# Optimization experiments

Measured on AMD Instinct MI355X. Metric: run time of the kernel, lower is better.

Reference implementation:

```python
import jax, jax.numpy as jnp
import numpy as np

ALPHA1 = 0.1   # rank margin
ALPHA2 = 5.0   # penalty scale when violated
ALPHA3 = 10.0  # sigmoid sharpness
ALPHA_OTHER = 0.5  # floor for top-k threshold


def setup_inputs() -> dict:
    key = jax.random.key(0)
    B, C, L, S = 4096, 9605, 8, 50  # batch, classes, whitelist labels, classes per label
    k1, k2, k3 = jax.random.split(key, 3)
    x = jax.random.normal(k1, (B, C), dtype=jnp.float32)
    # sparse multi-label binarized targets (~10 positives/sample)
    y = (jax.random.uniform(k2, (B, C)) < 0.001).astype(jnp.float32)
    y_neg = (jax.random.uniform(k3, (B, C)) < 0.001).astype(jnp.float32)
    # disjoint per-label whitelist class index sets -> [L, C] boolean masks
    rng = np.random.default_rng(0)
    idx = rng.choice(C, size=L * S, replace=False).reshape(L, S)
    wl = np.zeros((L, C), dtype=bool)
    wl[np.arange(L)[:, None], idx] = True
    return {"x": x, "y": y, "y_neg": y_neg, "wl_mask": jnp.asarray(wl)}


def reference(x, y, y_neg, wl_mask):
    # x, y, y_neg: [B, C]; wl_mask: [L, C] bool. Returns scalar loss_rank_all.sum().
    # (The per-element BCE `loss` tensor and find_gt_whitelist(y_neg) in the
    #  original are dead code w.r.t. the returned value and are omitted.)
    xs = jax.nn.sigmoid(x)                                   # [B, C]
    wl_f = wl_mask.astype(x.dtype)                           # [L, C]
    # gt label present iff sum of y over that label's whitelist indices > 0
    gt_mask = (y @ wl_f.T) > 0                               # [B, L]
    has_gt = jnp.any(gt_mask, axis=1)                        # [B]
    first_gt = jnp.argmax(gt_mask, axis=1)                   # [B] first gt label
    # x_sorted[15] (16th largest) via top_k instead of full sort
    top16 = jax.lax.top_k(xs, 16)[0][:, 15]                  # [B]
    thres = jnp.maximum(top16, ALPHA_OTHER)                  # [B]
    # ---- branch: no gt whitelist label ----
    union = jnp.any(wl_mask, axis=0)                         # [C]
    x2_no = jnp.max(jnp.where(union[None, :], xs, -jnp.inf), axis=1)
    x1_no = thres
    # ---- branch: has gt whitelist label ----
    samp_mask = wl_mask[first_gt]                            # [B, C]
    x1_gt = jnp.max(jnp.where(samp_mask, xs, -jnp.inf), axis=1)
    L = wl_mask.shape[0]
    # faithful to original: indexes xs at LABEL positions 0..L-1, init 0
    non_gt = jnp.max(jnp.where(~gt_mask, xs[:, :L], 0.0), axis=1, initial=0.0)
    x2_gt = jnp.maximum(non_gt, thres)
    # ---- select branch and apply our_rank_loss ----
    x1 = jnp.where(has_gt, x1_gt, x1_no)
    x2 = jnp.where(has_gt, x2_gt, x2_no)
    d = x2 - x1 + ALPHA1
    sig = jax.nn.sigmoid(ALPHA3 * d)
    rank = jnp.where(d > 0, ALPHA2 * sig, sig)
    return jnp.sum(rank)
```

## Files before the change

kernel.cpp:

```cpp
#include <hip/hip_runtime.h>
#include <stdint.h>

#define BLOCK 512
#define NW 5
#define CAP 512
#define LISTCAP 1024
#define WS_LIST 8
#define WS_ROUT 4096
static constexpr int LBL = 8;

#define A1 0.1f
#define A2 5.0f
#define A3 10.0f

__device__ __forceinline__ unsigned f2key(float f) {
  unsigned u = __float_as_uint(f);
  return (u & 0x80000000u) ? ~u : (u | 0x80000000u);
}
__device__ __forceinline__ float key2f(unsigned k) {
  unsigned u = (k & 0x80000000u) ? (k & 0x7FFFFFFFu) : ~k;
  return __uint_as_float(u);
}
__device__ __forceinline__ float sigm(float v) { return 1.0f / (1.0f + __expf(-v)); }

__global__ void detect_kernel(const unsigned char* __restrict__ wl, int total,
                              int* __restrict__ ws) {
  int i = blockIdx.x * 256 + threadIdx.x;
  if (i < total && (i & 3) != 0 && wl[i] == 1) atomicOr(&ws[1], 1);
}

__global__ void build_kernel(const unsigned char* __restrict__ wl, int C, int total,
                             int* __restrict__ ws) {
  int i = blockIdx.x * 256 + threadIdx.x;
  if (i >= total) return;
  bool v = ws[1] ? (wl[i] != 0) : (((const int*)wl)[i] != 0);
  if (v) {
    int p = atomicAdd(&ws[0], 1);
    if (p < LISTCAP) ws[WS_LIST + p] = ((i / C) << 16) | (i % C);
  }
}

__global__ __launch_bounds__(BLOCK, 8) void rank_kernel(
    const float* __restrict__ x, const float* __restrict__ y,
    const int* __restrict__ ws, float* __restrict__ rout, int C) {
  __shared__ unsigned hist[2048];
  __shared__ unsigned buf[CAP];
  __shared__ float wtop2[BLOCK / 64];
  __shared__ unsigned wtot[BLOCK / 64];
  __shared__ unsigned lmaxk[LBL];
  __shared__ float smL[LBL];
  __shared__ unsigned gtbits, bufcnt, s_seld, s_selk, s_selc, s_key;

  int tid = threadIdx.x;
  int row = blockIdx.x;
  long long base = (long long)row * C;
  const float* __restrict__ xr = x + base;
  const float* __restrict__ yr = y + base;

  int s = (int)((4 - (base & 3)) & 3);
  int nv = (C - s) >> 2;
  int tail0 = s + 4 * nv;
  int nrem = C - 4 * nv;

  const float4* __restrict__ xv4 = (const float4*)(xr + s);
  float4 f[NW];
  bool hv[NW];
#pragma unroll
  for (int t = 0; t < NW; ++t) {
    int i = tid + t * BLOCK;
    hv[t] = (i < nv);
    f[t] = hv[t] ? xv4[i] : make_float4(-INFINITY, -INFINITY, -INFINITY, -INFINITY);
  }
  float tailv = -INFINITY;
  bool havet = false;
  if (tid < nrem) {
    int c = (tid < s) ? tid : tail0 + (tid - s);
    tailv = xr[c];
    havet = true;
  }
  if (tid < LBL) smL[tid] = xr[tid];
  int e0 = ws[WS_LIST + tid];
  int e1 = ws[WS_LIST + BLOCK + tid];
  float xg0 = 0.0f, yg0 = 0.0f, xg1 = 0.0f, yg1 = 0.0f;
  if (e0 != -1) { int c = e0 & 0xFFFF; xg0 = xr[c]; yg0 = yr[c]; }
  if (e1 != -1) { int c = e1 & 0xFFFF; xg1 = xr[c]; yg1 = yr[c]; }

  if (tid < LBL) lmaxk[tid] = 0u;
  if (tid == 0) { gtbits = 0u; bufcnt = 0u; }
  __syncthreads();

  if (e0 != -1) {
    int l = e0 >> 16;
    atomicMax(&lmaxk[l], f2key(xg0));
    if (yg0 != 0.0f) atomicOr(&gtbits, 1u << l);
  }
  if (e1 != -1) {
    int l = e1 >> 16;
    atomicMax(&lmaxk[l], f2key(xg1));
    if (yg1 != 0.0f) atomicOr(&gtbits, 1u << l);
  }

  float tmax = tailv;
#pragma unroll
  for (int t = 0; t < NW; ++t)
    tmax = fmaxf(tmax, fmaxf(fmaxf(f[t].x, f[t].y), fmaxf(f[t].z, f[t].w)));

  float a1 = tmax, a2 = -INFINITY;
#pragma unroll
  for (int st = 1; st < 64; st <<= 1) {
    float b1 = __shfl_xor(a1, st, 64);
    float b2 = __shfl_xor(a2, st, 64);
    float m = fminf(a1, b1);
    float o = (a1 >= b1) ? a2 : b2;
    a1 = fmaxf(a1, b1);
    a2 = fmaxf(m, o);
  }
  int w = tid >> 6;
  if ((tid & 63) == 0) wtop2[w] = a2;
  __syncthreads();
  float p = wtop2[0];
#pragma unroll
  for (int i = 1; i < BLOCK / 64; ++i) p = fminf(p, wtop2[i]);

#pragma unroll
  for (int t = 0; t < NW; ++t) {
    if (f[t].x >= p) { unsigned q = atomicAdd(&bufcnt, 1u); if (q < CAP) buf[q] = f2key(f[t].x); }
    if (f[t].y >= p) { unsigned q = atomicAdd(&bufcnt, 1u); if (q < CAP) buf[q] = f2key(f[t].y); }
    if (f[t].z >= p) { unsigned q = atomicAdd(&bufcnt, 1u); if (q < CAP) buf[q] = f2key(f[t].z); }
    if (f[t].w >= p) { unsigned q = atomicAdd(&bufcnt, 1u); if (q < CAP) buf[q] = f2key(f[t].w); }
  }
  if (havet && tailv >= p) { unsigned q = atomicAdd(&bufcnt, 1u); if (q < CAP) buf[q] = f2key(tailv); }
  __syncthreads();

  unsigned selkey = 0u;
  int bc = (int)bufcnt;
  if (bc >= 16 && bc <= CAP) {
    if (tid < 64) {
      for (int i = tid; i < bc; i += 64) {
        unsigned mk = buf[i];
        int g = 0, e2 = 0;
        for (int j = 0; j < bc; ++j) {
          unsigned bk = buf[j];
          g += (bk > mk);
          e2 += (bk == mk);
        }
        if (g < 16 && 16 <= g + e2) s_key = mk;
      }
    }
    __syncthreads();
    selkey = s_key;
  } else {
    unsigned prefix = 0, pmask = 0;
    int k = 16;
    bool done = false;
    const int SHa[3] = {21, 10, 0};
    const int WIDa[3] = {11, 11, 10};
    for (int lev = 0; lev < 3 && !done; ++lev) {
      int shift = SHa[lev];
      int nb = 1 << WIDa[lev];
      unsigned bmask = (unsigned)nb - 1u;
      for (int i = tid; i < nb; i += BLOCK) hist[i] = 0;
      if (tid == 0) bufcnt = 0;
      __syncthreads();
#pragma unroll
      for (int t = 0; t < NW; ++t)
        if (hv[t]) {
          unsigned kk[4] = {f2key(f[t].x), f2key(f[t].y), f2key(f[t].z), f2key(f[t].w)};
#pragma unroll
          for (int e = 0; e < 4; ++e)
            if ((kk[e] & pmask) == prefix) atomicAdd(&hist[(kk[e] >> shift) & bmask], 1u);
        }
      if (havet) {
        unsigned tk = f2key(tailv);
        if ((tk & pmask) == prefix) atomicAdd(&hist[(tk >> shift) & bmask], 1u);
      }
      __syncthreads();
      int bpt = nb / BLOCK;
      int b0 = tid * bpt;
      unsigned cs = 0;
      for (int b = 0; b < bpt; ++b) cs += hist[b0 + b];
      unsigned v = cs;
      int lane = tid & 63;
#pragma unroll
      for (int st = 1; st < 64; st <<= 1) {
        unsigned tv = __shfl_down(v, st, 64);
        if (lane + st < 64) v += tv;
      }
      int w2 = tid >> 6;
      if (lane == 0) wtot[w2] = v;
      __syncthreads();
      unsigned above = 0;
      for (int ww = w2 + 1; ww < BLOCK / 64; ++ww) above += wtot[ww];
      unsigned S_incl = v + above;
      unsigned S_excl = S_incl - cs;
      if (S_excl < (unsigned)k && (unsigned)k <= S_incl) {
        int kk2 = k - (int)S_excl;
        int d = b0 + bpt - 1;
        for (; d > b0; --d) {
          int cb = (int)hist[d];
          if (kk2 <= cb) break;
          kk2 -= cb;
        }
        s_seld = (unsigned)d;
        s_selk = (unsigned)kk2;
        s_selc = hist[d];
      }
      __syncthreads();
      prefix |= s_seld << shift;
      pmask |= bmask << shift;
      k = (int)s_selk;
      unsigned selc = s_selc;
      if (lev == 2) {
        selkey = prefix;
        done = true;
      } else if (selc <= (unsigned)CAP) {
#pragma unroll
        for (int t = 0; t < NW; ++t)
          if (hv[t]) {
            unsigned kk[4] = {f2key(f[t].x), f2key(f[t].y), f2key(f[t].z), f2key(f[t].w)};
#pragma unroll
            for (int e = 0; e < 4; ++e)
              if ((kk[e] & pmask) == prefix) {
                unsigned q = atomicAdd(&bufcnt, 1u);
                if (q < CAP) buf[q] = kk[e];
              }
          }
        if (havet) {
          unsigned tk = f2key(tailv);
          if ((tk & pmask) == prefix) {
            unsigned q = atomicAdd(&bufcnt, 1u);
            if (q < CAP) buf[q] = tk;
          }
        }
        __syncthreads();
        int bc2 = (int)bufcnt;
        if (bc2 > CAP) bc2 = CAP;
        unsigned mk = (tid < bc2) ? buf[tid] : 0u;
        int g = 0, e2 = 0;
        for (int j = 0; j < bc2; ++j) {
          unsigned bk = buf[j];
          g += (bk > mk);
          e2 += (bk == mk);
        }
        if (tid < bc2 && g < k && k <= g + e2) s_key = mk;
        __syncthreads();
        selkey = s_key;
        done = true;
      }
    }
  }

  if (tid == 0) {
    float x16 = key2f(selkey);
    float thres = sigm(fmaxf(x16, 0.0f));
    unsigned gb = gtbits;
    float x1, x2;
    if (gb) {
      int first = __ffs((int)gb) - 1;
      x1 = sigm(key2f(lmaxk[first]));
      float ng = 0.0f;
      for (int l = 0; l < LBL; ++l)
        if (!((gb >> l) & 1)) ng = fmaxf(ng, sigm(smL[l]));
      x2 = fmaxf(ng, thres);
    } else {
      unsigned um = 0;
      for (int l = 0; l < LBL; ++l) um = um > lmaxk[l] ? um : lmaxk[l];
      x1 = thres;
      x2 = sigm(key2f(um));
    }
    float dd = x2 - x1 + A1;
    float sg = 1.0f / (1.0f + __expf(-A3 * dd));
    rout[row] = (dd > 0.0f) ? A2 * sg : sg;
  }
}

__global__ __launch_bounds__(256) void reduce_kernel(const float* __restrict__ rin,
                                                     float* __restrict__ out, int B) {
  __shared__ float smr[256];
  float acc = 0.0f;
  for (int i = threadIdx.x; i < B; i += 256) acc += rin[i];
  smr[threadIdx.x] = acc;
  __syncthreads();
  for (int st = 128; st > 0; st >>= 1) {
    if (threadIdx.x < st) smr[threadIdx.x] += smr[threadIdx.x + st];
    __syncthreads();
  }
  if (threadIdx.x == 0) out[0] = smr[0];
}

extern "C" void kernel_launch(void* const* d_in, const int* in_sizes, int n_in,
                              void* d_out, int out_size, void* d_ws, size_t ws_size,
                              hipStream_t stream) {
  const float* x = (const float*)d_in[0];
  const float* y = (const float*)d_in[1];
  const unsigned char* wl = (const unsigned char*)d_in[3];

  int C = in_sizes[3] / LBL;
  int B = in_sizes[0] / C;
  int total = LBL * C;
  int* ws = (int*)d_ws;

  hipMemsetAsync(ws, 0, WS_LIST * 4, stream);
  hipMemsetAsync(ws + WS_LIST, 0xFF, (size_t)LISTCAP * 4, stream);
  int nbs = (total + 255) / 256;
  hipLaunchKernelGGL(detect_kernel, dim3(nbs), dim3(256), 0, stream, wl, total, ws);
  hipLaunchKernelGGL(build_kernel, dim3(nbs), dim3(256), 0, stream, wl, C, total, ws);

  hipLaunchKernelGGL(rank_kernel, dim3(B), dim3(BLOCK), 0, stream, x, y, ws,
                     (float*)(ws + WS_ROUT), C);
  hipLaunchKernelGGL(reduce_kernel, dim3(1), dim3(256), 0, stream,
                     (const float*)(ws + WS_ROUT), (float*)d_out, B);
}
```

Baseline: 72.11 us.

## Process four rows per block with double-buffered register prefetch

Each block now handles four rows instead of one. The next row's x values are prefetched into registers while the current row is being processed, so global-memory latency overlaps with compute. Some barriers become a custom waitcnt plus s_barrier, and the whitelist list capacity grows so entries beyond the first block-width are handled in a loop. In exchange, register pressure rises with two row buffers live at once, which may cut occupancy, and the grid shrinks to a quarter of its former size.

After: 202.5 us. 181% more time.

```diff
diff --git a/kernel.cpp b/kernel.cpp
--- a/kernel.cpp
+++ b/kernel.cpp
@@ -4,9 +4,10 @@
 #define BLOCK 512
 #define NW 5
 #define CAP 512
-#define LISTCAP 1024
+#define LISTCAP 4096
 #define WS_LIST 8
-#define WS_ROUT 4096
+#define WS_ROUT 8192
+#define RPB 4
 static constexpr int LBL = 8;
 
 #define A1 0.1f
@@ -22,6 +23,10 @@
   return __uint_as_float(u);
 }
 __device__ __forceinline__ float sigm(float v) { return 1.0f / (1.0f + __expf(-v)); }
+
+__device__ __forceinline__ void bar_lds() {
+  asm volatile("s_waitcnt lgkmcnt(0)\n\ts_barrier" ::: "memory");
+}
 
 __global__ void detect_kernel(const unsigned char* __restrict__ wl, int total,
                               int* __restrict__ ws) {
@@ -40,9 +45,16 @@
   }
 }
 
+struct RowBuf {
+  float4 f[NW];
+  float tailv;
+  float xg, yg;
+  float sm8;
+};
+
 __global__ __launch_bounds__(BLOCK, 8) void rank_kernel(
     const float* __restrict__ x, const float* __restrict__ y,
-    const int* __restrict__ ws, float* __restrict__ rout, int C) {
+    const int* __restrict__ ws, float* __restrict__ rout, int C, int B) {
   __shared__ unsigned hist[2048];
   __shared__ unsigned buf[CAP];
   __shared__ float wtop2[BLOCK / 64];
@@ -52,225 +64,254 @@
   __shared__ unsigned gtbits, bufcnt, s_seld, s_selk, s_selc, s_key;
 
   int tid = threadIdx.x;
-  int row = blockIdx.x;
-  long long base = (long long)row * C;
-  const float* __restrict__ xr = x + base;
-  const float* __restrict__ yr = y + base;
-
-  int s = (int)((4 - (base & 3)) & 3);
-  int nv = (C - s) >> 2;
-  int tail0 = s + 4 * nv;
-  int nrem = C - 4 * nv;
-
-  const float4* __restrict__ xv4 = (const float4*)(xr + s);
-  float4 f[NW];
-  bool hv[NW];
-#pragma unroll
-  for (int t = 0; t < NW; ++t) {
-    int i = tid + t * BLOCK;
-    hv[t] = (i < nv);
-    f[t] = hv[t] ? xv4[i] : make_float4(-INFINITY, -INFINITY, -INFINITY, -INFINITY);
-  }
-  float tailv = -INFINITY;
-  bool havet = false;
-  if (tid < nrem) {
-    int c = (tid < s) ? tid : tail0 + (tid - s);
-    tailv = xr[c];
-    havet = true;
-  }
-  if (tid < LBL) smL[tid] = xr[tid];
   int e0 = ws[WS_LIST + tid];
-  int e1 = ws[WS_LIST + BLOCK + tid];
-  float xg0 = 0.0f, yg0 = 0.0f, xg1 = 0.0f, yg1 = 0.0f;
-  if (e0 != -1) { int c = e0 & 0xFFFF; xg0 = xr[c]; yg0 = yr[c]; }
-  if (e1 != -1) { int c = e1 & 0xFFFF; xg1 = xr[c]; yg1 = yr[c]; }
-
-  if (tid < LBL) lmaxk[tid] = 0u;
-  if (tid == 0) { gtbits = 0u; bufcnt = 0u; }
-  __syncthreads();
-
-  if (e0 != -1) {
-    int l = e0 >> 16;
-    atomicMax(&lmaxk[l], f2key(xg0));
-    if (yg0 != 0.0f) atomicOr(&gtbits, 1u << l);
-  }
-  if (e1 != -1) {
-    int l = e1 >> 16;
-    atomicMax(&lmaxk[l], f2key(xg1));
-    if (yg1 != 0.0f) atomicOr(&gtbits, 1u << l);
-  }
-
-  float tmax = tailv;
-#pragma unroll
-  for (int t = 0; t < NW; ++t)
-    tmax = fmaxf(tmax, fmaxf(fmaxf(f[t].x, f[t].y), fmaxf(f[t].z, f[t].w)));
-
-  float a1 = tmax, a2 = -INFINITY;
-#pragma unroll
-  for (int st = 1; st < 64; st <<= 1) {
-    float b1 = __shfl_xor(a1, st, 64);
-    float b2 = __shfl_xor(a2, st, 64);
-    float m = fminf(a1, b1);
-    float o = (a1 >= b1) ? a2 : b2;
-    a1 = fmaxf(a1, b1);
-    a2 = fmaxf(m, o);
-  }
-  int w = tid >> 6;
-  if ((tid & 63) == 0) wtop2[w] = a2;
-  __syncthreads();
-  float p = wtop2[0];
-#pragma unroll
-  for (int i = 1; i < BLOCK / 64; ++i) p = fminf(p, wtop2[i]);
-
-#pragma unroll
-  for (int t = 0; t < NW; ++t) {
-    if (f[t].x >= p) { unsigned q = atomicAdd(&bufcnt, 1u); if (q < CAP) buf[q] = f2key(f[t].x); }
-    if (f[t].y >= p) { unsigned q = atomicAdd(&bufcnt, 1u); if (q < CAP) buf[q] = f2key(f[t].y); }
-    if (f[t].z >= p) { unsigned q = atomicAdd(&bufcnt, 1u); if (q < CAP) buf[q] = f2key(f[t].z); }
-    if (f[t].w >= p) { unsigned q = atomicAdd(&bufcnt, 1u); if (q < CAP) buf[q] = f2key(f[t].w); }
-  }
-  if (havet && tailv >= p) { unsigned q = atomicAdd(&bufcnt, 1u); if (q < CAP) buf[q] = f2key(tailv); }
-  __syncthreads();
-
-  unsigned selkey = 0u;
-  int bc = (int)bufcnt;
-  if (bc >= 16 && bc <= CAP) {
-    if (tid < 64) {
-      for (int i = tid; i < bc; i += 64) {
-        unsigned mk = buf[i];
-        int g = 0, e2 = 0;
-        for (int j = 0; j < bc; ++j) {
-          unsigned bk = buf[j];
-          g += (bk > mk);
-          e2 += (bk == mk);
-        }
-        if (g < 16 && 16 <= g + e2) s_key = mk;
+  int cnt = ws[0];
+  if (cnt > LISTCAP) cnt = LISTCAP;
+  int row0 = blockIdx.x * RPB;
+
+  auto prefetch = [&](RowBuf& rb, int row) {
+    long long base = (long long)row * C;
+    const float* __restrict__ xr = x + base;
+    const float* __restrict__ yr = y + base;
+    int s = (int)((4 - (base & 3)) & 3);
+    int nv = (C - s) >> 2;
+    int tail0 = s + 4 * nv;
+    int nrem = C - 4 * nv;
+    const float4* __restrict__ xv4 = (const float4*)(xr + s);
+#pragma unroll
+    for (int t = 0; t < NW; ++t) {
+      int i = tid + t * BLOCK;
+      rb.f[t] = (i < nv) ? xv4[i]
+                         : make_float4(-INFINITY, -INFINITY, -INFINITY, -INFINITY);
+    }
+    rb.tailv = -INFINITY;
+    if (tid < nrem) {
+      int c = (tid < s) ? tid : tail0 + (tid - s);
+      rb.tailv = xr[c];
+    }
+    rb.sm8 = (tid < LBL) ? xr[tid] : 0.0f;
+    rb.xg = 0.0f;
+    rb.yg = 0.0f;
+    if (e0 != -1) {
+      int c = e0 & 0xFFFF;
+      rb.xg = xr[c];
+      rb.yg = yr[c];
+    }
+  };
+
+  auto process = [&](const RowBuf& rb, int row) {
+    long long base = (long long)row * C;
+    const float* __restrict__ xr = x + base;
+    const float* __restrict__ yr = y + base;
+    int s = (int)((4 - (base & 3)) & 3);
+    int nv = (C - s) >> 2;
+    int nrem = C - 4 * nv;
+    bool havet = (tid < nrem);
+
+    bar_lds();
+    if (tid < LBL) lmaxk[tid] = 0u;
+    if (tid == 0) { gtbits = 0u; bufcnt = 0u; }
+    bar_lds();
+
+    if (e0 != -1) {
+      int l = e0 >> 16;
+      atomicMax(&lmaxk[l], f2key(rb.xg));
+      if (rb.yg != 0.0f) atomicOr(&gtbits, 1u << l);
+    }
+    for (int j = BLOCK + tid; j < cnt; j += BLOCK) {
+      int e = ws[WS_LIST + j];
+      int c = e & 0xFFFF, l = e >> 16;
+      atomicMax(&lmaxk[l], f2key(xr[c]));
+      if (yr[c] != 0.0f) atomicOr(&gtbits, 1u << l);
+    }
+    if (tid < LBL) smL[tid] = rb.sm8;
+
+    float tmax = rb.tailv;
+#pragma unroll
+    for (int t = 0; t < NW; ++t)
+      tmax = fmaxf(tmax, fmaxf(fmaxf(rb.f[t].x, rb.f[t].y), fmaxf(rb.f[t].z, rb.f[t].w)));
+
+    float a1v = tmax, a2v = -INFINITY;
+#pragma unroll
+    for (int st = 1; st < 64; st <<= 1) {
+      float b1f = __shfl_xor(a1v, st, 64);
+      float b2f = __shfl_xor(a2v, st, 64);
+      float mn = fminf(a1v, b1f);
+      float ot = (a1v >= b1f) ? a2v : b2f;
+      a1v = fmaxf(a1v, b1f);
+      a2v = fmaxf(mn, ot);
+    }
+    int w = tid >> 6;
+    if ((tid & 63) == 0) wtop2[w] = a2v;
+    bar_lds();
+    float p = wtop2[0];
+#pragma unroll
+    for (int i = 1; i < BLOCK / 64; ++i) p = fminf(p, wtop2[i]);
+
+#pragma unroll
+    for (int t = 0; t < NW; ++t) {
+      if (rb.f[t].x >= p) { unsigned q = atomicAdd(&bufcnt, 1u); if (q < CAP) buf[q] = f2key(rb.f[t].x); }
+      if (rb.f[t].y >= p) { unsigned q = atomicAdd(&bufcnt, 1u); if (q < CAP) buf[q] = f2key(rb.f[t].y); }
+      if (rb.f[t].z >= p) { unsigned q = atomicAdd(&bufcnt, 1u); if (q < CAP) buf[q] = f2key(rb.f[t].z); }
+      if (rb.f[t].w >= p) { unsigned q = atomicAdd(&bufcnt, 1u); if (q < CAP) buf[q] = f2key(rb.f[t].w); }
+    }
+    if (havet && rb.tailv >= p) { unsigned q = atomicAdd(&bufcnt, 1u); if (q < CAP) buf[q] = f2key(rb.tailv); }
+    bar_lds();
+
+    unsigned selkey = 0u;
+    int bc = (int)bufcnt;
+    if (bc >= 16 && bc <= CAP) {
+      if (tid < 64) {
+        for (int i = tid; i < bc; i += 64) {
+          unsigned mk = buf[i];
+          int g = 0, e2 = 0;
+          for (int j = 0; j < bc; ++j) {
+            unsigned bk = buf[j];
+            g += (bk > mk);
+            e2 += (bk == mk);
+          }
+          if (g < 16 && 16 <= g + e2) s_key = mk;
+        }
       }
-    }
-    __syncthreads();
-    selkey = s_key;
-  } else {
-    unsigned prefix = 0, pmask = 0;
-    int k = 16;
-    bool done = false;
-    const int SHa[3] = {21, 10, 0};
-    const int WIDa[3] = {11, 11, 10};
-    for (int lev = 0; lev < 3 && !done; ++lev) {
-      int shift = SHa[lev];
-      int nb = 1 << WIDa[lev];
-      unsigned bmask = (unsigned)nb - 1u;
-      for (int i = tid; i < nb; i += BLOCK) hist[i] = 0;
-      if (tid == 0) bufcnt = 0;
-      __syncthreads();
-#pragma unroll
-      for (int t = 0; t < NW; ++t)
-        if (hv[t]) {
-          unsigned kk[4] = {f2key(f[t].x), f2key(f[t].y), f2key(f[t].z), f2key(f[t].w)};
-#pragma unroll
-          for (int e = 0; e < 4; ++e)
-            if ((kk[e] & pmask) == prefix) atomicAdd(&hist[(kk[e] >> shift) & bmask], 1u);
-        }
-      if (havet) {
-        unsigned tk = f2key(tailv);
-        if ((tk & pmask) == prefix) atomicAdd(&hist[(tk >> shift) & bmask], 1u);
+      bar_lds();
+      selkey = s_key;
+    } else {
+      unsigned prefix = 0, pmask = 0;
+      int k = 16;
+      bool done = false;
+      const int SHa[3] = {21, 10, 0};
+      const int WIDa[3] = {11, 11, 10};
+      for (int lev = 0; lev < 3 && !done; ++lev) {
+        int shift = SHa[lev];
+        int nb = 1 << WIDa[lev];
+        unsigned bmask = (unsigned)nb - 1u;
+        for (int i = tid; i < nb; i += BLOCK) hist[i] = 0;
+        if (tid == 0) bufcnt = 0;
+        __syncthreads();
+#pragma unroll
+        for (int t = 0; t < NW; ++t) {
+          int i = tid + t * BLOCK;
+          if (i < nv) {
+            unsigned kk[4] = {f2key(rb.f[t].x), f2key(rb.f[t].y), f2key(rb.f[t].z), f2key(rb.f[t].w)};
+#pragma unroll
+            for (int e = 0; e < 4; ++e)
+              if ((kk[e] & pmask) == prefix) atomicAdd(&hist[(kk[e] >> shift) & bmask], 1u);
+          }
+        }
+        if (havet) {
+          unsigned tk = f2key(rb.tailv);
+          if ((tk & pmask) == prefix) atomicAdd(&hist[(tk >> shift) & bmask], 1u);
+        }
+        __syncthreads();
+        int bpt = nb / BLOCK;
+        int b0i = tid * bpt;
+        unsigned cs = 0;
+        for (int b = 0; b < bpt; ++b) cs += hist[b0i + b];
+        unsigned v = cs;
+        int lane = tid & 63;
+#pragma unroll
+        for (int st = 1; st < 64; st <<= 1) {
+          unsigned tv = __shfl_down(v, st, 64);
+          if (lane + st < 64) v += tv;
+        }
+        int w2 = tid >> 6;
+        if (lane == 0) wtot[w2] = v;
+        __syncthreads();
+        unsigned above = 0;
+        for (int ww = w2 + 1; ww < BLOCK / 64; ++ww) above += wtot[ww];
+        unsigned S_incl = v + above;
+        unsigned S_excl = S_incl - cs;
+        if (S_excl < (unsigned)k && (unsigned)k <= S_incl) {
+          int kk2 = k - (int)S_excl;
+          int d = b0i + bpt - 1;
+          for (; d > b0i; --d) {
+            int cb = (int)hist[d];
+            if (kk2 <= cb) break;
+            kk2 -= cb;
+          }
+          s_seld = (unsigned)d;
+          s_selk = (unsigned)kk2;
+          s_selc = hist[d];
+        }
+        __syncthreads();
+        prefix |= s_seld << shift;
+        pmask |= bmask << shift;
+        k = (int)s_selk;
+        unsigned selc = s_selc;
+        if (lev == 2) {
+          selkey = prefix;
+          done = true;
+        } else if (selc <= (unsigned)CAP) {
+#pragma unroll
+          for (int t = 0; t < NW; ++t) {
+            int i = tid + t * BLOCK;
+            if (i < nv) {
+              unsigned kk[4] = {f2key(rb.f[t].x), f2key(rb.f[t].y), f2key(rb.f[t].z), f2key(rb.f[t].w)};
+#pragma unroll
+              for (int e = 0; e < 4; ++e)
+                if ((kk[e] & pmask) == prefix) {
+                  unsigned q = atomicAdd(&bufcnt, 1u);
+                  if (q < CAP) buf[q] = kk[e];
+                }
+            }
+          }
+          if (havet) {
+            unsigned tk = f2key(rb.tailv);
+            if ((tk & pmask) == prefix) {
+              unsigned q = atomicAdd(&bufcnt, 1u);
+              if (q < CAP) buf[q] = tk;
+            }
+          }
+          __syncthreads();
+          int bc2 = (int)bufcnt;
+          if (bc2 > CAP) bc2 = CAP;
+          unsigned mk = (tid < bc2) ? buf[tid] : 0u;
+          int g = 0, e2 = 0;
+          for (int j = 0; j < bc2; ++j) {
+            unsigned bk = buf[j];
+            g += (bk > mk);
+            e2 += (bk == mk);
+          }
+          if (tid < bc2 && g < k && k <= g + e2) s_key = mk;
+          __syncthreads();
+          selkey = s_key;
+          done = true;
+        }
       }
-      __syncthreads();
-      int bpt = nb / BLOCK;
-      int b0 = tid * bpt;
-      unsigned cs = 0;
-      for (int b = 0; b < bpt; ++b) cs += hist[b0 + b];
-      unsigned v = cs;
-      int lane = tid & 63;
-#pragma unroll
-      for (int st = 1; st < 64; st <<= 1) {
-        unsigned tv = __shfl_down(v, st, 64);
-        if (lane + st < 64) v += tv;
+    }
+
+    if (tid == 0) {
+      float x16 = key2f(selkey);
+      float thres = sigm(fmaxf(x16, 0.0f));
+      unsigned gb = gtbits;
+      float x1, x2;
+      if (gb) {
+        int first = __ffs((int)gb) - 1;
+        x1 = sigm(key2f(lmaxk[first]));
+        float ng = 0.0f;
+        for (int l = 0; l < LBL; ++l)
+          if (!((gb >> l) & 1)) ng = fmaxf(ng, sigm(smL[l]));
+        x2 = fmaxf(ng, thres);
+      } else {
+        unsigned um = 0;
+        for (int l = 0; l < LBL; ++l) um = um > lmaxk[l] ? um : lmaxk[l];
+        x1 = thres;
+        x2 = sigm(key2f(um));
       }
-      int w2 = tid >> 6;
-      if (lane == 0) wtot[w2] = v;
-      __syncthreads();
-      unsigned above = 0;
-      for (int ww = w2 + 1; ww < BLOCK / 64; ++ww) above += wtot[ww];
-      unsigned S_incl = v + above;
-      unsigned S_excl = S_incl - cs;
-      if (S_excl < (unsigned)k && (unsigned)k <= S_incl) {
-        int kk2 = k - (int)S_excl;
-        int d = b0 + bpt - 1;
-        for (; d > b0; --d) {
-          int cb = (int)hist[d];
-          if (kk2 <= cb) break;
-          kk2 -= cb;
-        }
-        s_seld = (unsigned)d;
-        s_selk = (unsigned)kk2;
-        s_selc = hist[d];
-      }
-      __syncthreads();
-      prefix |= s_seld << shift;
-      pmask |= bmask << shift;
-      k = (int)s_selk;
-      unsigned selc = s_selc;
-      if (lev == 2) {
-        selkey = prefix;
-        done = true;
-      } else if (selc <= (unsigned)CAP) {
-#pragma unroll
-        for (int t = 0; t < NW; ++t)
-          if (hv[t]) {
-            unsigned kk[4] = {f2key(f[t].x), f2key(f[t].y), f2key(f[t].z), f2key(f[t].w)};
-#pragma unroll
-            for (int e = 0; e < 4; ++e)
-              if ((kk[e] & pmask) == prefix) {
-                unsigned q = atomicAdd(&bufcnt, 1u);
-                if (q < CAP) buf[q] = kk[e];
-              }
-          }
-        if (havet) {
-          unsigned tk = f2key(tailv);
-          if ((tk & pmask) == prefix) {
-            unsigned q = atomicAdd(&bufcnt, 1u);
-            if (q < CAP) buf[q] = tk;
-          }
-        }
-        __syncthreads();
-        int bc2 = (int)bufcnt;
-        if (bc2 > CAP) bc2 = CAP;
-        unsigned mk = (tid < bc2) ? buf[tid] : 0u;
-        int g = 0, e2 = 0;
-        for (int j = 0; j < bc2; ++j) {
-          unsigned bk = buf[j];
-          g += (bk > mk);
-          e2 += (bk == mk);
-        }
-        if (tid < bc2 && g < k && k <= g + e2) s_key = mk;
-        __syncthreads();
-        selkey = s_key;
-        done = true;
-      }
-    }
-  }
-
-  if (tid == 0) {
-    float x16 = key2f(selkey);
-    float thres = sigm(fmaxf(x16, 0.0f));
-    unsigned gb = gtbits;
-    float x1, x2;
-    if (gb) {
-      int first = __ffs((int)gb) - 1;
-      x1 = sigm(key2f(lmaxk[first]));
-      float ng = 0.0f;
-      for (int l = 0; l < LBL; ++l)
-        if (!((gb >> l) & 1)) ng = fmaxf(ng, sigm(smL[l]));
-      x2 = fmaxf(ng, thres);
-    } else {
-      unsigned um = 0;
-      for (int l = 0; l < LBL; ++l) um = um > lmaxk[l] ? um : lmaxk[l];
-      x1 = thres;
-      x2 = sigm(key2f(um));
-    }
-    float dd = x2 - x1 + A1;
-    float sg = 1.0f / (1.0f + __expf(-A3 * dd));
-    rout[row] = (dd > 0.0f) ? A2 * sg : sg;
+      float dd = x2 - x1 + A1;
+      float sg = 1.0f / (1.0f + __expf(-A3 * dd));
+      rout[row] = (dd > 0.0f) ? A2 * sg : sg;
+    }
+  };
+
+  RowBuf bufA, bufB;
+  if (row0 < B) prefetch(bufA, row0);
+#pragma unroll
+  for (int r = 0; r < RPB; r += 2) {
+    if (row0 + r + 1 < B) prefetch(bufB, row0 + r + 1);
+    if (row0 + r < B) process(bufA, row0 + r);
+    if (row0 + r + 2 < B) prefetch(bufA, row0 + r + 2);
+    if (row0 + r + 1 < B) process(bufB, row0 + r + 1);
   }
 }
 
@@ -306,8 +347,9 @@
   hipLaunchKernelGGL(detect_kernel, dim3(nbs), dim3(256), 0, stream, wl, total, ws);
   hipLaunchKernelGGL(build_kernel, dim3(nbs), dim3(256), 0, stream, wl, C, total, ws);
 
-  hipLaunchKernelGGL(rank_kernel, dim3(B), dim3(BLOCK), 0, stream, x, y, ws,
-                     (float*)(ws + WS_ROUT), C);
+  int nblk = (B + RPB - 1) / RPB;
+  hipLaunchKernelGGL(rank_kernel, dim3(nblk), dim3(BLOCK), 0, stream, x, y, ws,
+                     (float*)(ws + WS_ROUT), C, B);
   hipLaunchKernelGGL(reduce_kernel, dim3(1), dim3(256), 0, stream,
                      (const float*)(ws + WS_ROUT), (float*)d_out, B);
 }
```

## Map whitelist entries to owning threads to reuse register-resident x values

Applied to the files above, without the earlier changes.

Replaces the flat whitelist index list with a per-alignment owner table: each whitelist column is assigned to the thread that already holds it in registers, so its x value is taken from the loaded float4 instead of a separate scattered global load. Only y is gathered for owned entries; tail and overflow columns are handled through small side tables. This cuts per-row scattered global loads of x and moves the label max/gt atomics after the first barrier. The cost is a more complex build kernel with four alignment variants and a larger workspace memset.

New measurement: 142.7 us. 97.9% more time.

```diff
diff --git a/kernel.cpp b/kernel.cpp
--- a/kernel.cpp
+++ b/kernel.cpp
@@ -4,9 +4,11 @@
 #define BLOCK 512
 #define NW 5
 #define CAP 512
-#define LISTCAP 1024
-#define WS_LIST 8
-#define WS_ROUT 4096
+#define OT0 64
+#define CNT0 4160
+#define OVF0 6208
+#define HT0 8256
+#define WS_ROUT 12288
 static constexpr int LBL = 8;
 
 #define A1 0.1f
@@ -22,6 +24,11 @@
   return __uint_as_float(u);
 }
 __device__ __forceinline__ float sigm(float v) { return 1.0f / (1.0f + __expf(-v)); }
+
+__device__ __forceinline__ float pick(const float4* f, int t, int e) {
+  float4 v = (t == 0) ? f[0] : (t == 1) ? f[1] : (t == 2) ? f[2] : (t == 3) ? f[3] : f[4];
+  return (e == 0) ? v.x : (e == 1) ? v.y : (e == 2) ? v.z : v.w;
+}
 
 __global__ void detect_kernel(const unsigned char* __restrict__ wl, int total,
                               int* __restrict__ ws) {
@@ -29,14 +36,33 @@
   if (i < total && (i & 3) != 0 && wl[i] == 1) atomicOr(&ws[1], 1);
 }
 
-__global__ void build_kernel(const unsigned char* __restrict__ wl, int C, int total,
-                             int* __restrict__ ws) {
+__global__ void build_owner(const unsigned char* __restrict__ wl, int C, int total,
+                            int* __restrict__ ws) {
   int i = blockIdx.x * 256 + threadIdx.x;
   if (i >= total) return;
   bool v = ws[1] ? (wl[i] != 0) : (((const int*)wl)[i] != 0);
-  if (v) {
-    int p = atomicAdd(&ws[0], 1);
-    if (p < LISTCAP) ws[WS_LIST + p] = ((i / C) << 16) | (i % C);
+  if (!v) return;
+  int l = i / C, c = i % C;
+  if (c < 4) ws[HT0 + c] = l + 1;
+  if (c >= C - 4) ws[HT0 + 4 + (c - (C - 4))] = l + 1;
+#pragma unroll
+  for (int s = 0; s < 4; ++s) {
+    if (c < s) continue;
+    int w = (c - s) >> 2;
+    if (w >= ((C - s) >> 2)) continue;
+    int owner = w & (BLOCK - 1);
+    int t = w >> 9;
+    int e = (c - s) & 3;
+    unsigned entry = 0x8000u | ((unsigned)t << 12) | ((unsigned)e << 10) |
+                     ((unsigned)l << 7);
+    int pos = atomicAdd(&ws[CNT0 + s * BLOCK + owner], 1);
+    if (pos < 4) {
+      atomicOr((unsigned*)&ws[OT0 + s * 1024 + 2 * owner + (pos >> 1)],
+               entry << ((pos & 1) * 16));
+    } else {
+      int q = atomicAdd(&ws[2 + s], 1);
+      if (q < 512) ws[OVF0 + s * 512 + q] = (l << 16) | c;
+    }
   }
 }
 
@@ -64,64 +90,89 @@
 
   const float4* __restrict__ xv4 = (const float4*)(xr + s);
   float4 f[NW];
-  bool hv[NW];
 #pragma unroll
   for (int t = 0; t < NW; ++t) {
     int i = tid + t * BLOCK;
-    hv[t] = (i < nv);
-    f[t] = hv[t] ? xv4[i] : make_float4(-INFINITY, -INFINITY, -INFINITY, -INFINITY);
-  }
-  float tailv = -INFINITY;
+    f[t] = (i < nv) ? xv4[i]
+                    : make_float4(-INFINITY, -INFINITY, -INFINITY, -INFINITY);
+  }
+  float tailv = -INFINITY, tyv = 0.0f;
   bool havet = false;
+  int tlab = -1;
   if (tid < nrem) {
-    int c = (tid < s) ? tid : tail0 + (tid - s);
-    tailv = xr[c];
+    int tc = (tid < s) ? tid : tail0 + (tid - s);
+    tailv = xr[tc];
     havet = true;
+    int hv2 = (tc < 4) ? ws[HT0 + tc] : ws[HT0 + 4 + (tc - (C - 4))];
+    if (hv2 > 0) { tlab = hv2 - 1; tyv = yr[tc]; }
   }
   if (tid < LBL) smL[tid] = xr[tid];
-  int e0 = ws[WS_LIST + tid];
-  int e1 = ws[WS_LIST + BLOCK + tid];
-  float xg0 = 0.0f, yg0 = 0.0f, xg1 = 0.0f, yg1 = 0.0f;
-  if (e0 != -1) { int c = e0 & 0xFFFF; xg0 = xr[c]; yg0 = yr[c]; }
-  if (e1 != -1) { int c = e1 & 0xFFFF; xg1 = xr[c]; yg1 = yr[c]; }
+
+  uint2 ot = *(const uint2*)&ws[OT0 + s * 1024 + 2 * tid];
+  unsigned en[4] = {ot.x & 0xFFFFu, ot.x >> 16, ot.y & 0xFFFFu, ot.y >> 16};
+  int tt[4], ee[4], lb[4];
+  bool va[4];
+  float yg[4];
+#pragma unroll
+  for (int k = 0; k < 4; ++k) {
+    va[k] = (en[k] & 0x8000u) != 0;
+    tt[k] = (en[k] >> 12) & 7;
+    ee[k] = (en[k] >> 10) & 3;
+    lb[k] = (en[k] >> 7) & 7;
+    int c = s + 4 * (tt[k] * BLOCK + tid) + ee[k];
+    yg[k] = va[k] ? yr[c] : 0.0f;
+  }
+  int ovfc = ws[2 + s];
+  if (ovfc > 512) ovfc = 512;
+  int olab = -1;
+  float oxv = 0.0f, oyv = 0.0f;
+  if (tid < ovfc) {
+    int e = ws[OVF0 + s * 512 + tid];
+    int c = e & 0xFFFF;
+    olab = e >> 16;
+    oxv = xr[c];
+    oyv = yr[c];
+  }
 
   if (tid < LBL) lmaxk[tid] = 0u;
   if (tid == 0) { gtbits = 0u; bufcnt = 0u; }
-  __syncthreads();
-
-  if (e0 != -1) {
-    int l = e0 >> 16;
-    atomicMax(&lmaxk[l], f2key(xg0));
-    if (yg0 != 0.0f) atomicOr(&gtbits, 1u << l);
-  }
-  if (e1 != -1) {
-    int l = e1 >> 16;
-    atomicMax(&lmaxk[l], f2key(xg1));
-    if (yg1 != 0.0f) atomicOr(&gtbits, 1u << l);
-  }
 
   float tmax = tailv;
 #pragma unroll
   for (int t = 0; t < NW; ++t)
     tmax = fmaxf(tmax, fmaxf(fmaxf(f[t].x, f[t].y), fmaxf(f[t].z, f[t].w)));
-
-  float a1 = tmax, a2 = -INFINITY;
+  float a1v = tmax, a2v = -INFINITY;
 #pragma unroll
   for (int st = 1; st < 64; st <<= 1) {
-    float b1 = __shfl_xor(a1, st, 64);
-    float b2 = __shfl_xor(a2, st, 64);
-    float m = fminf(a1, b1);
-    float o = (a1 >= b1) ? a2 : b2;
-    a1 = fmaxf(a1, b1);
-    a2 = fmaxf(m, o);
+    float b1f = __shfl_xor(a1v, st, 64);
+    float b2f = __shfl_xor(a2v, st, 64);
+    float mn = fminf(a1v, b1f);
+    float ot2 = (a1v >= b1f) ? a2v : b2f;
+    a1v = fmaxf(a1v, b1f);
+    a2v = fmaxf(mn, ot2);
   }
   int w = tid >> 6;
-  if ((tid & 63) == 0) wtop2[w] = a2;
+  if ((tid & 63) == 0) wtop2[w] = a2v;
   __syncthreads();
+
+#pragma unroll
+  for (int k = 0; k < 4; ++k)
+    if (va[k]) {
+      atomicMax(&lmaxk[lb[k]], f2key(pick(f, tt[k], ee[k])));
+      if (yg[k] != 0.0f) atomicOr(&gtbits, 1u << lb[k]);
+    }
+  if (olab >= 0) {
+    atomicMax(&lmaxk[olab], f2key(oxv));
+    if (oyv != 0.0f) atomicOr(&gtbits, 1u << olab);
+  }
+  if (havet && tlab >= 0) {
+    atomicMax(&lmaxk[tlab], f2key(tailv));
+    if (tyv != 0.0f) atomicOr(&gtbits, 1u << tlab);
+  }
+
   float p = wtop2[0];
 #pragma unroll
   for (int i = 1; i < BLOCK / 64; ++i) p = fminf(p, wtop2[i]);
-
 #pragma unroll
   for (int t = 0; t < NW; ++t) {
     if (f[t].x >= p) { unsigned q = atomicAdd(&bufcnt, 1u); if (q < CAP) buf[q] = f2key(f[t].x); }
@@ -163,22 +214,24 @@
       if (tid == 0) bufcnt = 0;
       __syncthreads();
 #pragma unroll
-      for (int t = 0; t < NW; ++t)
-        if (hv[t]) {
+      for (int t = 0; t < NW; ++t) {
+        int i = tid + t * BLOCK;
+        if (i < nv) {
           unsigned kk[4] = {f2key(f[t].x), f2key(f[t].y), f2key(f[t].z), f2key(f[t].w)};
 #pragma unroll
           for (int e = 0; e < 4; ++e)
             if ((kk[e] & pmask) == prefix) atomicAdd(&hist[(kk[e] >> shift) & bmask], 1u);
         }
+      }
       if (havet) {
         unsigned tk = f2key(tailv);
         if ((tk & pmask) == prefix) atomicAdd(&hist[(tk >> shift) & bmask], 1u);
       }
       __syncthreads();
       int bpt = nb / BLOCK;
-      int b0 = tid * bpt;
+      int b0i = tid * bpt;
       unsigned cs = 0;
-      for (int b = 0; b < bpt; ++b) cs += hist[b0 + b];
+      for (int b = 0; b < bpt; ++b) cs += hist[b0i + b];
       unsigned v = cs;
       int lane = tid & 63;
 #pragma unroll
@@ -195,8 +248,8 @@
       unsigned S_excl = S_incl - cs;
       if (S_excl < (unsigned)k && (unsigned)k <= S_incl) {
         int kk2 = k - (int)S_excl;
-        int d = b0 + bpt - 1;
-        for (; d > b0; --d) {
+        int d = b0i + bpt - 1;
+        for (; d > b0i; --d) {
           int cb = (int)hist[d];
           if (kk2 <= cb) break;
           kk2 -= cb;
@@ -215,8 +268,9 @@
         done = true;
       } else if (selc <= (unsigned)CAP) {
 #pragma unroll
-        for (int t = 0; t < NW; ++t)
-          if (hv[t]) {
+        for (int t = 0; t < NW; ++t) {
+          int i = tid + t * BLOCK;
+          if (i < nv) {
             unsigned kk[4] = {f2key(f[t].x), f2key(f[t].y), f2key(f[t].z), f2key(f[t].w)};
 #pragma unroll
             for (int e = 0; e < 4; ++e)
@@ -225,6 +279,7 @@
                 if (q < CAP) buf[q] = kk[e];
               }
           }
+        }
         if (havet) {
           unsigned tk = f2key(tailv);
           if ((tk & pmask) == prefix) {
@@ -300,11 +355,10 @@
   int total = LBL * C;
   int* ws = (int*)d_ws;
 
-  hipMemsetAsync(ws, 0, WS_LIST * 4, stream);
-  hipMemsetAsync(ws + WS_LIST, 0xFF, (size_t)LISTCAP * 4, stream);
+  hipMemsetAsync(ws, 0, (size_t)(HT0 + 8) * 4, stream);
   int nbs = (total + 255) / 256;
   hipLaunchKernelGGL(detect_kernel, dim3(nbs), dim3(256), 0, stream, wl, total, ws);
-  hipLaunchKernelGGL(build_kernel, dim3(nbs), dim3(256), 0, stream, wl, C, total, ws);
+  hipLaunchKernelGGL(build_owner, dim3(nbs), dim3(256), 0, stream, wl, C, total, ws);
 
   hipLaunchKernelGGL(rank_kernel, dim3(B), dim3(BLOCK), 0, stream, x, y, ws,
                      (float*)(ws + WS_ROUT), C);
```
